# Kernel optimization log

Hardware: AMD Instinct MI355X
Metric: run time of the kernel (lower is better)

Reference implementation:

```python
import jax, jax.numpy as jnp
import numpy as np


def gin_conv(x, src, dst, W, b, num_nodes):
    # PyG GINConv with eps=0: nn((1+eps)*x + sum_{j in N(i)} x_j)
    agg = jax.ops.segment_sum(x[src], dst, num_segments=num_nodes)
    return (x + agg) @ W + b


def setup_inputs() -> dict:
    key = jax.random.key(0)
    ks = jax.random.split(key, 16)
    N, E, F, G = 100000, 3200000, 64, 512
    x = jax.random.normal(ks[0], (N, F), dtype=jnp.float32)
    edge_index = jax.random.randint(ks[1], (2, E), 0, N, dtype=jnp.int64)
    batch = jnp.sort(jax.random.randint(ks[2], (N,), 0, G, dtype=jnp.int64))

    def lin(k, fi, fo):
        return jax.random.normal(k, (fi, fo), dtype=jnp.float32) / np.sqrt(fi)

    return {
        "x": x, "edge_index": edge_index, "batch": batch, "num_graphs": G,
        "W1": lin(ks[3], F, 32), "b1": jnp.zeros((32,), jnp.float32),
        "W2": lin(ks[4], 32, 64), "b2": jnp.zeros((64,), jnp.float32),
        "W3": lin(ks[5], 64, 64), "b3": jnp.zeros((64,), jnp.float32),
        "Wf1": lin(ks[6], 64, 64), "bf1": jnp.zeros((64,), jnp.float32),
        "Wf2": lin(ks[7], 64, 32), "bf2": jnp.zeros((32,), jnp.float32),
        "Wf3": lin(ks[8], 32, 1), "bf3": jnp.zeros((1,), jnp.float32),
    }


def reference(x, edge_index, batch, num_graphs,
              W1, b1, W2, b2, W3, b3, Wf1, bf1, Wf2, bf2, Wf3, bf3):
    N = x.shape[0]
    src, dst = edge_index[0], edge_index[1]
    h = jax.nn.elu(gin_conv(x, src, dst, W1, b1, N))
    h = jax.nn.elu(gin_conv(h, src, dst, W2, b2, N))
    h = jax.nn.elu(gin_conv(h, src, dst, W3, b3, N))
    # scatter_mean pooling over graphs
    sums = jax.ops.segment_sum(h, batch, num_segments=num_graphs)
    cnts = jax.ops.segment_sum(jnp.ones((N,), h.dtype), batch, num_segments=num_graphs)
    g = sums / jnp.maximum(cnts, 1.0)[:, None]
    g = jax.nn.elu(g @ Wf1 + bf1)
    g = jax.nn.elu(g @ Wf2 + bf2)
    g = g @ Wf3 + bf3
    return g.reshape(-1)
```

## Files before the change

### kernel.cpp

```cpp
#include <hip/hip_runtime.h>
#include <hip/hip_bf16.h>


typedef float f4 __attribute__((ext_vector_type(4)));

#define NCHUNK 512
#define MAXK 1024

__device__ __forceinline__ float elu_f(float x) {
  return x > 0.0f ? x : expm1f(x);
}

__device__ __forceinline__ float rl(float v, int q) {
  return __int_as_float(__builtin_amdgcn_readlane(__float_as_int(v), q));
}

__device__ __forceinline__ unsigned short f2bf(float f) {
  unsigned int u = __float_as_uint(f);
  u = (u + 0x7FFFu + ((u >> 16) & 1u)) >> 16;
  return (unsigned short)u;
}

__device__ __forceinline__ void acc_add8(float* a, const uint4 w) {
  a[0] += __uint_as_float(w.x << 16);
  a[1] += __uint_as_float(w.x & 0xffff0000u);
  a[2] += __uint_as_float(w.y << 16);
  a[3] += __uint_as_float(w.y & 0xffff0000u);
  a[4] += __uint_as_float(w.z << 16);
  a[5] += __uint_as_float(w.z & 0xffff0000u);
  a[6] += __uint_as_float(w.w << 16);
  a[7] += __uint_as_float(w.w & 0xffff0000u);
}


__global__ __launch_bounds__(256) void cvt_bf16_kernel(
    const float* __restrict__ in, unsigned short* __restrict__ out, int n4) {
  typedef unsigned short us4 __attribute__((ext_vector_type(4)));
  const int stride = gridDim.x * blockDim.x;
  for (int i = blockIdx.x * blockDim.x + threadIdx.x; i < n4; i += stride) {
    const f4 v = *reinterpret_cast<const f4*>(in + (long long)i * 4);
    us4 o;
    o.x = f2bf(v.x); o.y = f2bf(v.y); o.z = f2bf(v.z); o.w = f2bf(v.w);
    *reinterpret_cast<us4*>(out + (long long)i * 4) = o;
  }
}


__global__ __launch_bounds__(256) void bucket_hist_kernel(
    const int* __restrict__ dst, int* __restrict__ bhist, int E, int K, int chunk) {
  __shared__ int h[MAXK];
  for (int k = threadIdx.x; k < K; k += 256) h[k] = 0;
  __syncthreads();
  const int base = blockIdx.x * chunk;
  const int end = min(E, base + chunk);
  for (int e = base + threadIdx.x; e < end; e += 256)
    atomicAdd(&h[dst[e] >> 7], 1);
  __syncthreads();
  int* row = bhist + (long long)blockIdx.x * K;
  for (int k = threadIdx.x; k < K; k += 256) row[k] = h[k];
}

__global__ __launch_bounds__(NCHUNK) void chunk_scan_kernel(
    const int* __restrict__ bhist, int* __restrict__ cursors,
    int* __restrict__ btot, int K) {
  const int k = blockIdx.x;
  const int t = threadIdx.x;
  const int lane = t & 63;
  const int wv = t >> 6;
  const int own = bhist[(long long)t * K + k];
  int v = own;
#pragma unroll
  for (int off = 1; off < 64; off <<= 1) {
    int u = __shfl_up(v, off, 64);
    if (lane >= off) v += u;
  }
  __shared__ int wsum[8];
  __shared__ int wpre[8];
  if (lane == 63) wsum[wv] = v;
  __syncthreads();
  if (t == 0) {
    int p = 0;
#pragma unroll
    for (int w = 0; w < 8; ++w) { wpre[w] = p; p += wsum[w]; }
  }
  __syncthreads();
  v += wpre[wv];
  cursors[(long long)t * K + k] = v - own;
  if (t == NCHUNK - 1) btot[k] = v;
}

__global__ __launch_bounds__(1024) void bucket_scan_kernel(
    const int* __restrict__ btot, int* __restrict__ bstart, int K) {
  __shared__ int s[1024];
  const int t = threadIdx.x;
  const int own = (t < K) ? btot[t] : 0;
  s[t] = own;
  __syncthreads();
#pragma unroll
  for (int off = 1; off < 1024; off <<= 1) {
    int v = (t >= off) ? s[t - off] : 0;
    __syncthreads();
    s[t] += v;
    __syncthreads();
  }
  if (t < K) bstart[t] = s[t] - own;
  if (t == K - 1) bstart[K] = s[t];
}

__global__ __launch_bounds__(256) void bucket_scatter_kernel(
    const int* __restrict__ src, const int* __restrict__ dst,
    const int* __restrict__ cursors, const int* __restrict__ bstart,
    int* __restrict__ packed, int E, int K, int chunk) {
  __shared__ int cur[MAXK];
  const int c = blockIdx.x;
  for (int k = threadIdx.x; k < K; k += 256)
    cur[k] = cursors[(long long)c * K + k] + bstart[k];
  __syncthreads();
  const int base = c * chunk;
  const int end = min(E, base + chunk);
  for (int e = base + threadIdx.x; e < end; e += 256) {
    const int d = dst[e];
    const int k = d >> 7;
    const int p = atomicAdd(&cur[k], 1);
    packed[p] = ((d & 127) << 18) | src[e];
  }
}

__global__ __launch_bounds__(256) void bucket_sort_kernel(
    const int* __restrict__ packed, const int* __restrict__ bstart,
    int* __restrict__ rowptr, int* __restrict__ eidx, int N, int E, int K) {
  __shared__ int hcnt[128];
  __shared__ int ccur[128];
  __shared__ int wtot;
  const int k = blockIdx.x;
  const int t = threadIdx.x;
  const int lane = t & 63;
  const int n0 = k << 7;
  const int e0 = bstart[k];
  const int e1 = bstart[k + 1];
  if (t < 128) hcnt[t] = 0;
  __syncthreads();
  for (int e = e0 + t; e < e1; e += 256)
    atomicAdd(&hcnt[packed[e] >> 18], 1);
  __syncthreads();
  int v = 0, own = 0;
  if (t < 128) {
    own = hcnt[t];
    v = own;
#pragma unroll
    for (int off = 1; off < 64; off <<= 1) {
      int u = __shfl_up(v, off, 64);
      if (lane >= off) v += u;
    }
  }
  if (t == 63) wtot = v;
  __syncthreads();
  if (t >= 64 && t < 128) v += wtot;
  if (t < 128) {
    const int excl = v - own;
    ccur[t] = excl;
    if (n0 + t < N) rowptr[n0 + t] = e0 + excl;
  }
  if (k == 0 && t == 0) rowptr[N] = E;
  __syncthreads();
  for (int e = e0 + t; e < e1; e += 256) {
    const int w = packed[e];
    const int dl = w >> 18;
    const int p = atomicAdd(&ccur[dl], 1);
    eidx[e0 + p] = w & 0x3FFFF;
  }
}


template <int FO>
__global__ __launch_bounds__(256) void gin_layer64_kernel(
    const unsigned short* __restrict__ h, const int* __restrict__ rowptr,
    const int* __restrict__ eidx, const float* __restrict__ W,
    const float* __restrict__ b, unsigned short* __restrict__ out, int N) {
  const int lane = threadIdx.x & 63;
  const int grp = lane >> 3;
  const int li = lane & 7;
  const int wid = blockIdx.x * (blockDim.x >> 6) + (threadIdx.x >> 6);
  const int nw = gridDim.x * (blockDim.x >> 6);
  const int fo = lane & (FO - 1);
  float wcol[(FO == 32) ? 32 : 64];
  if constexpr (FO == 32) {
    const int kbase = (lane >> 5) * 32;
#pragma unroll
    for (int j = 0; j < 32; ++j) wcol[j] = W[(kbase + j) * 32 + fo];
  } else {
#pragma unroll
    for (int k = 0; k < 64; ++k) wcol[k] = W[k * 64 + fo];
  }
  const float bias = b[fo];

  for (int n = wid; n < N; n += nw) {
    const int r0 = rowptr[n];
    const int cnt = rowptr[n + 1] - r0;
    float a[8] = {0.f, 0.f, 0.f, 0.f, 0.f, 0.f, 0.f, 0.f};
    float a2[8] = {0.f, 0.f, 0.f, 0.f, 0.f, 0.f, 0.f, 0.f};
    int i = grp;
    for (; i + 8 < cnt; i += 16) {
      const int s0 = eidx[r0 + i];
      const int s1 = eidx[r0 + i + 8];
      const uint4 w0 = *reinterpret_cast<const uint4*>(h + (long long)s0 * 64 + li * 8);
      const uint4 w1 = *reinterpret_cast<const uint4*>(h + (long long)s1 * 64 + li * 8);
      acc_add8(a, w0);
      acc_add8(a2, w1);
    }
    if (i < cnt) {
      const int s = eidx[r0 + i];
      acc_add8(a, *reinterpret_cast<const uint4*>(h + (long long)s * 64 + li * 8));
    }
#pragma unroll
    for (int j = 0; j < 8; ++j) {
      a[j] += a2[j];
      a[j] += __shfl_xor(a[j], 8, 64);
      a[j] += __shfl_xor(a[j], 16, 64);
      a[j] += __shfl_xor(a[j], 32, 64);
    }
    acc_add8(a, *reinterpret_cast<const uint4*>(h + (long long)n * 64 + li * 8));
    if constexpr (FO == 32) {
      float o = (lane < 32) ? bias : 0.0f;
      const int pbase = (lane >> 5) * 16;
#pragma unroll
      for (int j = 0; j < 32; ++j) {
        const float av = __int_as_float(__builtin_amdgcn_ds_bpermute(
            pbase + (j >> 3) * 4, __float_as_int(a[j & 7])));
        o = fmaf(av, wcol[j], o);
      }
      o += __shfl_xor(o, 32, 64);
      if (lane < 32) out[(long long)n * 32 + lane] = f2bf(elu_f(o));
    } else {
      float o0 = bias, o1 = 0.0f;
#pragma unroll
      for (int k = 0; k < 64; k += 2) {
        o0 = fmaf(rl(a[k & 7], k >> 3), wcol[k], o0);
        o1 = fmaf(rl(a[(k + 1) & 7], (k + 1) >> 3), wcol[k + 1], o1);
      }
      out[(long long)n * 64 + lane] = f2bf(elu_f(o0 + o1));
    }
  }
}

__global__ __launch_bounds__(256) void gin_layer32_kernel(
    const unsigned short* __restrict__ h, const int* __restrict__ rowptr,
    const int* __restrict__ eidx, const float* __restrict__ W,
    const float* __restrict__ b, unsigned short* __restrict__ out, int N) {
  const int lane = threadIdx.x & 63;
  const int grp = lane >> 2;
  const int li = lane & 3;
  const int wid = blockIdx.x * (blockDim.x >> 6) + (threadIdx.x >> 6);
  const int nw = gridDim.x * (blockDim.x >> 6);
  float wcol[32];
#pragma unroll
  for (int k = 0; k < 32; ++k) wcol[k] = W[k * 64 + lane];
  const float bias = b[lane];

  for (int n = wid; n < N; n += nw) {
    const int r0 = rowptr[n];
    const int cnt = rowptr[n + 1] - r0;
    float a[8] = {0.f, 0.f, 0.f, 0.f, 0.f, 0.f, 0.f, 0.f};
    float a2[8] = {0.f, 0.f, 0.f, 0.f, 0.f, 0.f, 0.f, 0.f};
    int i = grp;
    for (; i + 16 < cnt; i += 32) {
      const int s0 = eidx[r0 + i];
      const int s1 = eidx[r0 + i + 16];
      const uint4 w0 = *reinterpret_cast<const uint4*>(h + (long long)s0 * 32 + li * 8);
      const uint4 w1 = *reinterpret_cast<const uint4*>(h + (long long)s1 * 32 + li * 8);
      acc_add8(a, w0);
      acc_add8(a2, w1);
    }
    if (i < cnt) {
      const int s = eidx[r0 + i];
      acc_add8(a, *reinterpret_cast<const uint4*>(h + (long long)s * 32 + li * 8));
    }
#pragma unroll
    for (int j = 0; j < 8; ++j) {
      a[j] += a2[j];
      a[j] += __shfl_xor(a[j], 4, 64);
      a[j] += __shfl_xor(a[j], 8, 64);
      a[j] += __shfl_xor(a[j], 16, 64);
      a[j] += __shfl_xor(a[j], 32, 64);
    }
    acc_add8(a, *reinterpret_cast<const uint4*>(h + (long long)n * 32 + li * 8));
    float o0 = bias, o1 = 0.0f;
#pragma unroll
    for (int k = 0; k < 32; k += 2) {
      o0 = fmaf(rl(a[k & 7], k >> 3), wcol[k], o0);
      o1 = fmaf(rl(a[(k + 1) & 7], (k + 1) >> 3), wcol[k + 1], o1);
    }
    out[(long long)n * 64 + lane] = f2bf(elu_f(o0 + o1));
  }
}


__global__ void pool_kernel(const unsigned short* __restrict__ h,
                            const int* __restrict__ batch,
                            float* __restrict__ sums,
                            float* __restrict__ cnts,
                            int N) {
  const int groupsPerBlock = blockDim.x >> 6;
  const int grp = blockIdx.x * groupsPerBlock + (threadIdx.x >> 6);
  const int ngrp = gridDim.x * groupsPerBlock;
  const int f = threadIdx.x & 63;
  const int chunk = (N + ngrp - 1) / ngrp;
  const int n0 = grp * chunk;
  const int n1 = min(N, n0 + chunk);
  if (n0 >= n1) return;
  int g = batch[n0];
  float acc = 0.0f;
  float cnt = 0.0f;
  for (int n = n0; n < n1; ++n) {
    const int bg = batch[n];
    if (bg != g) {
      atomicAdd(&sums[(long long)g * 64 + f], acc);
      if (f == 0) atomicAdd(&cnts[g], cnt);
      acc = 0.0f;
      cnt = 0.0f;
      g = bg;
    }
    acc += __uint_as_float((unsigned int)h[(long long)n * 64 + f] << 16);
    cnt += 1.0f;
  }
  atomicAdd(&sums[(long long)g * 64 + f], acc);
  if (f == 0) atomicAdd(&cnts[g], cnt);
}

__global__ void head_kernel(const float* __restrict__ sums,
                            const float* __restrict__ cnts,
                            const float* __restrict__ Wf1, const float* __restrict__ bf1,
                            const float* __restrict__ Wf2, const float* __restrict__ bf2,
                            const float* __restrict__ Wf3, const float* __restrict__ bf3,
                            float* __restrict__ out, int G) {
  __shared__ float s0[64];
  __shared__ float s1[64];
  __shared__ float s2[32];
  const int g = blockIdx.x;
  const int t = threadIdx.x;
  const float c = fmaxf(cnts[g], 1.0f);
  s0[t] = sums[(long long)g * 64 + t] / c;
  __syncthreads();
  float acc = bf1[t];
#pragma unroll
  for (int k = 0; k < 64; ++k) acc += s0[k] * Wf1[k * 64 + t];
  s1[t] = elu_f(acc);
  __syncthreads();
  if (t < 32) {
    float a2 = bf2[t];
#pragma unroll
    for (int k = 0; k < 64; ++k) a2 += s1[k] * Wf2[k * 32 + t];
    s2[t] = elu_f(a2) * Wf3[t];
  }
  __syncthreads();
  if (t == 0) {
    float r = bf3[0];
#pragma unroll
    for (int k = 0; k < 32; ++k) r += s2[k];
    out[g] = r;
  }
}

extern "C" void kernel_launch(void* const* d_in, const int* in_sizes, int n_in,
                              void* d_out, int out_size, void* d_ws, size_t ws_size,
                              hipStream_t stream) {
  const float* x   = (const float*)d_in[0];
  const int* ei    = (const int*)d_in[1];
  const int* batch = (const int*)d_in[2];
  const float* W1  = (const float*)d_in[4];
  const float* b1  = (const float*)d_in[5];
  const float* W2  = (const float*)d_in[6];
  const float* b2  = (const float*)d_in[7];
  const float* W3  = (const float*)d_in[8];
  const float* b3  = (const float*)d_in[9];
  const float* Wf1 = (const float*)d_in[10];
  const float* bf1 = (const float*)d_in[11];
  const float* Wf2 = (const float*)d_in[12];
  const float* bf2 = (const float*)d_in[13];
  const float* Wf3 = (const float*)d_in[14];
  const float* bf3 = (const float*)d_in[15];

  const int N = in_sizes[0] / 64;
  const int E = in_sizes[1] / 2;
  const int G = out_size;
  const int* src = ei;
  const int* dst = ei + E;
  const int K = (N + 127) >> 7;
  const int chunk = (E + NCHUNK - 1) / NCHUNK;

  char* ws = (char*)d_ws;
  size_t off = 0;
  auto alloc = [&](size_t bytes) -> void* {
    void* p = ws + off;
    off = (off + bytes + 255) & ~(size_t)255;
    return p;
  };
  int* bhist   = (int*)alloc((size_t)NCHUNK * K * 4);
  int* cursors = (int*)alloc((size_t)NCHUNK * K * 4);
  int* btot    = (int*)alloc((size_t)K * 4);
  int* bstart  = (int*)alloc((size_t)(K + 1) * 4);
  int* rowptr  = (int*)alloc((size_t)(N + 1) * 4);
  int* eidx    = (int*)alloc((size_t)E * 4);
  int* packed  = (int*)alloc((size_t)E * 4);
  unsigned short* xb = (unsigned short*)alloc((size_t)N * 64 * 2);
  unsigned short* hA = (unsigned short*)alloc((size_t)N * 64 * 2);
  unsigned short* hB = (unsigned short*)alloc((size_t)N * 64 * 2);
  float* sums  = (float*)alloc((size_t)G * 65 * 4);
  float* cnts  = sums + (size_t)G * 64;
  float* out   = (float*)d_out;

  cvt_bf16_kernel<<<1024, 256, 0, stream>>>(x, xb, N * 16);

  bucket_hist_kernel<<<NCHUNK, 256, 0, stream>>>(dst, bhist, E, K, chunk);
  chunk_scan_kernel<<<K, NCHUNK, 0, stream>>>(bhist, cursors, btot, K);
  bucket_scan_kernel<<<1, 1024, 0, stream>>>(btot, bstart, K);
  bucket_scatter_kernel<<<NCHUNK, 256, 0, stream>>>(src, dst, cursors, bstart,
                                                    packed, E, K, chunk);
  bucket_sort_kernel<<<K, 256, 0, stream>>>(packed, bstart, rowptr, eidx, N, E, K);

  gin_layer64_kernel<32><<<2048, 256, 0, stream>>>(xb, rowptr, eidx, W1, b1, hA, N);
  gin_layer32_kernel<<<2048, 256, 0, stream>>>(hA, rowptr, eidx, W2, b2, hB, N);
  gin_layer64_kernel<64><<<2048, 256, 0, stream>>>(hB, rowptr, eidx, W3, b3, hA, N);

  hipMemsetAsync(sums, 0, (size_t)G * 65 * 4, stream);
  pool_kernel<<<512, 256, 0, stream>>>(hA, batch, sums, cnts, N);
  head_kernel<<<G, 64, 0, stream>>>(sums, cnts, Wf1, bf1, Wf2, bf2, Wf3, bf3, out, G);
}
```

Before: 477.1 us.

## Partition edges by source tile so gather passes stay cache-resident

The CSR sort now orders each destination's edges by one of four source-node tiles and produces a 4x rowptr. The GIN layers process each tile in turn, with blocks owning fixed node ranges and keeping partial sums in shared memory between tiles. The goal is to keep the active slice of the source feature table resident in L2/LLC and cut random-gather misses. The cost is extra passes, block barriers, a shared-memory round-trip, and the loss of the dual-accumulator unrolling. The 32-feature layer also switches to 8 lanes of 4 features.

Result: slower. 790.1 us (+65.6%).

```diff
diff --git a/kernel.cpp b/kernel.cpp
--- a/kernel.cpp
+++ b/kernel.cpp
@@ -6,6 +6,7 @@
 
 #define NCHUNK 512
 #define MAXK 1024
+#define T_TILES 4
 
 __device__ __forceinline__ float elu_f(float x) {
   return x > 0.0f ? x : expm1f(x);
@@ -32,6 +33,17 @@
   a[7] += __uint_as_float(w.w & 0xffff0000u);
 }
 
+__device__ __forceinline__ void acc_add4(float* a, const uint2 w) {
+  a[0] += __uint_as_float(w.x << 16);
+  a[1] += __uint_as_float(w.x & 0xffff0000u);
+  a[2] += __uint_as_float(w.y << 16);
+  a[3] += __uint_as_float(w.y & 0xffff0000u);
+}
+
+__device__ __forceinline__ int tile_of(int srcn, float tszInv) {
+  return min(T_TILES - 1, (int)((float)srcn * tszInv));
+}
+
 
 __global__ __launch_bounds__(256) void cvt_bf16_kernel(
     const float* __restrict__ in, unsigned short* __restrict__ out, int n4) {
@@ -128,60 +140,72 @@
 
 __global__ __launch_bounds__(256) void bucket_sort_kernel(
     const int* __restrict__ packed, const int* __restrict__ bstart,
-    int* __restrict__ rowptr, int* __restrict__ eidx, int N, int E, int K) {
-  __shared__ int hcnt[128];
-  __shared__ int ccur[128];
-  __shared__ int wtot;
+    int* __restrict__ rowptr2, int* __restrict__ eidx, int N, int E, int K,
+    float tszInv) {
+  __shared__ int hcnt[512];
+  __shared__ int ccur[512];
+  __shared__ int wsum[4];
   const int k = blockIdx.x;
   const int t = threadIdx.x;
   const int lane = t & 63;
+  const int wv = t >> 6;
   const int n0 = k << 7;
   const int e0 = bstart[k];
   const int e1 = bstart[k + 1];
-  if (t < 128) hcnt[t] = 0;
-  __syncthreads();
-  for (int e = e0 + t; e < e1; e += 256)
-    atomicAdd(&hcnt[packed[e] >> 18], 1);
-  __syncthreads();
-  int v = 0, own = 0;
-  if (t < 128) {
-    own = hcnt[t];
-    v = own;
-#pragma unroll
-    for (int off = 1; off < 64; off <<= 1) {
-      int u = __shfl_up(v, off, 64);
-      if (lane >= off) v += u;
-    }
-  }
-  if (t == 63) wtot = v;
-  __syncthreads();
-  if (t >= 64 && t < 128) v += wtot;
-  if (t < 128) {
-    const int excl = v - own;
-    ccur[t] = excl;
-    if (n0 + t < N) rowptr[n0 + t] = e0 + excl;
-  }
-  if (k == 0 && t == 0) rowptr[N] = E;
+  hcnt[t] = 0;
+  hcnt[t + 256] = 0;
   __syncthreads();
   for (int e = e0 + t; e < e1; e += 256) {
     const int w = packed[e];
-    const int dl = w >> 18;
-    const int p = atomicAdd(&ccur[dl], 1);
-    eidx[e0 + p] = w & 0x3FFFF;
-  }
-}
-
-
-template <int FO>
-__global__ __launch_bounds__(256) void gin_layer64_kernel(
-    const unsigned short* __restrict__ h, const int* __restrict__ rowptr,
+    const int srcn = w & 0x3FFFF;
+    atomicAdd(&hcnt[(w >> 18) * T_TILES + tile_of(srcn, tszInv)], 1);
+  }
+  __syncthreads();
+  const int c0 = hcnt[2 * t];
+  const int c1 = hcnt[2 * t + 1];
+  const int own = c0 + c1;
+  int v = own;
+#pragma unroll
+  for (int off = 1; off < 64; off <<= 1) {
+    int u = __shfl_up(v, off, 64);
+    if (lane >= off) v += u;
+  }
+  if (lane == 63) wsum[wv] = v;
+  __syncthreads();
+  int pre = 0;
+#pragma unroll
+  for (int w = 0; w < 4; ++w) pre += (w < wv) ? wsum[w] : 0;
+  const int ex = pre + v - own;
+  ccur[2 * t] = ex;
+  ccur[2 * t + 1] = ex + c0;
+  const int key0 = 2 * t;
+  const int key1 = 2 * t + 1;
+  if (n0 + (key0 >> 2) < N) rowptr2[(n0 << 2) + key0] = e0 + ex;
+  if (n0 + (key1 >> 2) < N) rowptr2[(n0 << 2) + key1] = e0 + ex + c0;
+  if (k == 0 && t == 0) rowptr2[(long long)N << 2] = E;
+  __syncthreads();
+  for (int e = e0 + t; e < e1; e += 256) {
+    const int w = packed[e];
+    const int srcn = w & 0x3FFFF;
+    const int key = (w >> 18) * T_TILES + tile_of(srcn, tszInv);
+    const int p = atomicAdd(&ccur[key], 1);
+    eidx[e0 + p] = srcn;
+  }
+}
+
+
+template <int FO, int NPB>
+__global__ __launch_bounds__(256) void gin64_tiled_kernel(
+    const unsigned short* __restrict__ h, const int* __restrict__ rp2,
     const int* __restrict__ eidx, const float* __restrict__ W,
     const float* __restrict__ b, unsigned short* __restrict__ out, int N) {
+  __shared__ float accs[NPB][64];
   const int lane = threadIdx.x & 63;
+  const int wv = threadIdx.x >> 6;
   const int grp = lane >> 3;
   const int li = lane & 7;
-  const int wid = blockIdx.x * (blockDim.x >> 6) + (threadIdx.x >> 6);
-  const int nw = gridDim.x * (blockDim.x >> 6);
+  const int nb0 = blockIdx.x * NPB;
+  const int nEnd = min(N, nb0 + NPB);
   const int fo = lane & (FO - 1);
   float wcol[(FO == 32) ? 32 : 64];
   if constexpr (FO == 32) {
@@ -194,103 +218,125 @@
   }
   const float bias = b[fo];
 
-  for (int n = wid; n < N; n += nw) {
-    const int r0 = rowptr[n];
-    const int cnt = rowptr[n + 1] - r0;
-    float a[8] = {0.f, 0.f, 0.f, 0.f, 0.f, 0.f, 0.f, 0.f};
-    float a2[8] = {0.f, 0.f, 0.f, 0.f, 0.f, 0.f, 0.f, 0.f};
-    int i = grp;
-    for (; i + 8 < cnt; i += 16) {
-      const int s0 = eidx[r0 + i];
-      const int s1 = eidx[r0 + i + 8];
-      const uint4 w0 = *reinterpret_cast<const uint4*>(h + (long long)s0 * 64 + li * 8);
-      const uint4 w1 = *reinterpret_cast<const uint4*>(h + (long long)s1 * 64 + li * 8);
-      acc_add8(a, w0);
-      acc_add8(a2, w1);
+#pragma unroll 1
+  for (int tl = 0; tl < T_TILES; ++tl) {
+    for (int nn = nb0 + wv; nn < nEnd; nn += 4) {
+      float a[8];
+      if (tl > 0 && grp == 0) {
+        const f4 p0 = *reinterpret_cast<const f4*>(&accs[nn - nb0][li * 8]);
+        const f4 p1 = *reinterpret_cast<const f4*>(&accs[nn - nb0][li * 8 + 4]);
+        a[0] = p0.x; a[1] = p0.y; a[2] = p0.z; a[3] = p0.w;
+        a[4] = p1.x; a[5] = p1.y; a[6] = p1.z; a[7] = p1.w;
+      } else {
+#pragma unroll
+        for (int j = 0; j < 8; ++j) a[j] = 0.0f;
+      }
+      const int rb = (nn << 2) + tl;
+      const int r0 = rp2[rb];
+      const int r1 = rp2[rb + 1];
+      for (int i = r0 + grp; i < r1; i += 8) {
+        const int s = __builtin_nontemporal_load(&eidx[i]);
+        acc_add8(a, *reinterpret_cast<const uint4*>(h + (long long)s * 64 + li * 8));
+      }
+#pragma unroll
+      for (int j = 0; j < 8; ++j) {
+        a[j] += __shfl_xor(a[j], 8, 64);
+        a[j] += __shfl_xor(a[j], 16, 64);
+        a[j] += __shfl_xor(a[j], 32, 64);
+      }
+      if (tl < T_TILES - 1) {
+        if (grp == 0) {
+          f4 p0 = {a[0], a[1], a[2], a[3]};
+          f4 p1 = {a[4], a[5], a[6], a[7]};
+          *reinterpret_cast<f4*>(&accs[nn - nb0][li * 8]) = p0;
+          *reinterpret_cast<f4*>(&accs[nn - nb0][li * 8 + 4]) = p1;
+        }
+      } else {
+        acc_add8(a, *reinterpret_cast<const uint4*>(h + (long long)nn * 64 + li * 8));
+        if constexpr (FO == 32) {
+          float o = (lane < 32) ? bias : 0.0f;
+          const int pbase = (lane >> 5) * 16;
+#pragma unroll
+          for (int j = 0; j < 32; ++j) {
+            const float av = __int_as_float(__builtin_amdgcn_ds_bpermute(
+                pbase + (j >> 3) * 4, __float_as_int(a[j & 7])));
+            o = fmaf(av, wcol[j], o);
+          }
+          o += __shfl_xor(o, 32, 64);
+          if (lane < 32) out[(long long)nn * 32 + lane] = f2bf(elu_f(o));
+        } else {
+          float o0 = bias, o1 = 0.0f;
+#pragma unroll
+          for (int k2 = 0; k2 < 64; k2 += 2) {
+            o0 = fmaf(rl(a[k2 & 7], k2 >> 3), wcol[k2], o0);
+            o1 = fmaf(rl(a[(k2 + 1) & 7], (k2 + 1) >> 3), wcol[k2 + 1], o1);
+          }
+          out[(long long)nn * 64 + lane] = f2bf(elu_f(o0 + o1));
+        }
+      }
     }
-    if (i < cnt) {
-      const int s = eidx[r0 + i];
-      acc_add8(a, *reinterpret_cast<const uint4*>(h + (long long)s * 64 + li * 8));
-    }
-#pragma unroll
-    for (int j = 0; j < 8; ++j) {
-      a[j] += a2[j];
-      a[j] += __shfl_xor(a[j], 8, 64);
-      a[j] += __shfl_xor(a[j], 16, 64);
-      a[j] += __shfl_xor(a[j], 32, 64);
-    }
-    acc_add8(a, *reinterpret_cast<const uint4*>(h + (long long)n * 64 + li * 8));
-    if constexpr (FO == 32) {
-      float o = (lane < 32) ? bias : 0.0f;
-      const int pbase = (lane >> 5) * 16;
-#pragma unroll
-      for (int j = 0; j < 32; ++j) {
-        const float av = __int_as_float(__builtin_amdgcn_ds_bpermute(
-            pbase + (j >> 3) * 4, __float_as_int(a[j & 7])));
-        o = fmaf(av, wcol[j], o);
-      }
-      o += __shfl_xor(o, 32, 64);
-      if (lane < 32) out[(long long)n * 32 + lane] = f2bf(elu_f(o));
-    } else {
-      float o0 = bias, o1 = 0.0f;
-#pragma unroll
-      for (int k = 0; k < 64; k += 2) {
-        o0 = fmaf(rl(a[k & 7], k >> 3), wcol[k], o0);
-        o1 = fmaf(rl(a[(k + 1) & 7], (k + 1) >> 3), wcol[k + 1], o1);
-      }
-      out[(long long)n * 64 + lane] = f2bf(elu_f(o0 + o1));
-    }
-  }
-}
-
-__global__ __launch_bounds__(256) void gin_layer32_kernel(
-    const unsigned short* __restrict__ h, const int* __restrict__ rowptr,
+    __syncthreads();
+  }
+}
+
+template <int NPB>
+__global__ __launch_bounds__(256) void gin32_tiled_kernel(
+    const unsigned short* __restrict__ h, const int* __restrict__ rp2,
     const int* __restrict__ eidx, const float* __restrict__ W,
     const float* __restrict__ b, unsigned short* __restrict__ out, int N) {
+  __shared__ float accs[NPB][32];
   const int lane = threadIdx.x & 63;
-  const int grp = lane >> 2;
-  const int li = lane & 3;
-  const int wid = blockIdx.x * (blockDim.x >> 6) + (threadIdx.x >> 6);
-  const int nw = gridDim.x * (blockDim.x >> 6);
+  const int wv = threadIdx.x >> 6;
+  const int grp = lane >> 3;
+  const int li = lane & 7;
+  const int nb0 = blockIdx.x * NPB;
+  const int nEnd = min(N, nb0 + NPB);
   float wcol[32];
 #pragma unroll
   for (int k = 0; k < 32; ++k) wcol[k] = W[k * 64 + lane];
   const float bias = b[lane];
 
-  for (int n = wid; n < N; n += nw) {
-    const int r0 = rowptr[n];
-    const int cnt = rowptr[n + 1] - r0;
-    float a[8] = {0.f, 0.f, 0.f, 0.f, 0.f, 0.f, 0.f, 0.f};
-    float a2[8] = {0.f, 0.f, 0.f, 0.f, 0.f, 0.f, 0.f, 0.f};
-    int i = grp;
-    for (; i + 16 < cnt; i += 32) {
-      const int s0 = eidx[r0 + i];
-      const int s1 = eidx[r0 + i + 16];
-      const uint4 w0 = *reinterpret_cast<const uint4*>(h + (long long)s0 * 32 + li * 8);
-      const uint4 w1 = *reinterpret_cast<const uint4*>(h + (long long)s1 * 32 + li * 8);
-      acc_add8(a, w0);
-      acc_add8(a2, w1);
+#pragma unroll 1
+  for (int tl = 0; tl < T_TILES; ++tl) {
+    for (int nn = nb0 + wv; nn < nEnd; nn += 4) {
+      float a[4];
+      if (tl > 0 && grp == 0) {
+        const f4 p0 = *reinterpret_cast<const f4*>(&accs[nn - nb0][li * 4]);
+        a[0] = p0.x; a[1] = p0.y; a[2] = p0.z; a[3] = p0.w;
+      } else {
+#pragma unroll
+        for (int j = 0; j < 4; ++j) a[j] = 0.0f;
+      }
+      const int rb = (nn << 2) + tl;
+      const int r0 = rp2[rb];
+      const int r1 = rp2[rb + 1];
+      for (int i = r0 + grp; i < r1; i += 8) {
+        const int s = __builtin_nontemporal_load(&eidx[i]);
+        acc_add4(a, *reinterpret_cast<const uint2*>(h + (long long)s * 32 + li * 4));
+      }
+#pragma unroll
+      for (int j = 0; j < 4; ++j) {
+        a[j] += __shfl_xor(a[j], 8, 64);
+        a[j] += __shfl_xor(a[j], 16, 64);
+        a[j] += __shfl_xor(a[j], 32, 64);
+      }
+      if (tl < T_TILES - 1) {
+        if (grp == 0) {
+          f4 p0 = {a[0], a[1], a[2], a[3]};
+          *reinterpret_cast<f4*>(&accs[nn - nb0][li * 4]) = p0;
+        }
+      } else {
+        acc_add4(a, *reinterpret_cast<const uint2*>(h + (long long)nn * 32 + li * 4));
+        float o0 = bias, o1 = 0.0f;
+#pragma unroll
+        for (int k2 = 0; k2 < 32; k2 += 2) {
+          o0 = fmaf(rl(a[k2 & 3], k2 >> 2), wcol[k2], o0);
+          o1 = fmaf(rl(a[(k2 + 1) & 3], (k2 + 1) >> 2), wcol[k2 + 1], o1);
+        }
+        out[(long long)nn * 64 + lane] = f2bf(elu_f(o0 + o1));
+      }
     }
-    if (i < cnt) {
-      const int s = eidx[r0 + i];
-      acc_add8(a, *reinterpret_cast<const uint4*>(h + (long long)s * 32 + li * 8));
-    }
-#pragma unroll
-    for (int j = 0; j < 8; ++j) {
-      a[j] += a2[j];
-      a[j] += __shfl_xor(a[j], 4, 64);
-      a[j] += __shfl_xor(a[j], 8, 64);
-      a[j] += __shfl_xor(a[j], 16, 64);
-      a[j] += __shfl_xor(a[j], 32, 64);
-    }
-    acc_add8(a, *reinterpret_cast<const uint4*>(h + (long long)n * 32 + li * 8));
-    float o0 = bias, o1 = 0.0f;
-#pragma unroll
-    for (int k = 0; k < 32; k += 2) {
-      o0 = fmaf(rl(a[k & 7], k >> 3), wcol[k], o0);
-      o1 = fmaf(rl(a[(k + 1) & 7], (k + 1) >> 3), wcol[k + 1], o1);
-    }
-    out[(long long)n * 64 + lane] = f2bf(elu_f(o0 + o1));
+    __syncthreads();
   }
 }
 
@@ -387,6 +433,8 @@
   const int* dst = ei + E;
   const int K = (N + 127) >> 7;
   const int chunk = (E + NCHUNK - 1) / NCHUNK;
+  const int tsz = (N + T_TILES - 1) / T_TILES;
+  const float tszInv = 1.0f / (float)tsz;
 
   char* ws = (char*)d_ws;
   size_t off = 0;
@@ -399,7 +447,7 @@
   int* cursors = (int*)alloc((size_t)NCHUNK * K * 4);
   int* btot    = (int*)alloc((size_t)K * 4);
   int* bstart  = (int*)alloc((size_t)(K + 1) * 4);
-  int* rowptr  = (int*)alloc((size_t)(N + 1) * 4);
+  int* rowptr2 = (int*)alloc(((size_t)N * T_TILES + 1) * 4);
   int* eidx    = (int*)alloc((size_t)E * 4);
   int* packed  = (int*)alloc((size_t)E * 4);
   unsigned short* xb = (unsigned short*)alloc((size_t)N * 64 * 2);
@@ -416,11 +464,17 @@
   bucket_scan_kernel<<<1, 1024, 0, stream>>>(btot, bstart, K);
   bucket_scatter_kernel<<<NCHUNK, 256, 0, stream>>>(src, dst, cursors, bstart,
                                                     packed, E, K, chunk);
-  bucket_sort_kernel<<<K, 256, 0, stream>>>(packed, bstart, rowptr, eidx, N, E, K);
-
-  gin_layer64_kernel<32><<<2048, 256, 0, stream>>>(xb, rowptr, eidx, W1, b1, hA, N);
-  gin_layer32_kernel<<<2048, 256, 0, stream>>>(hA, rowptr, eidx, W2, b2, hB, N);
-  gin_layer64_kernel<64><<<2048, 256, 0, stream>>>(hB, rowptr, eidx, W3, b3, hA, N);
+  bucket_sort_kernel<<<K, 256, 0, stream>>>(packed, bstart, rowptr2, eidx,
+                                            N, E, K, tszInv);
+
+  {
+    const int npb1 = 56, g1 = (N + npb1 - 1) / npb1;
+    gin64_tiled_kernel<32, 56><<<g1, 256, 0, stream>>>(xb, rowptr2, eidx, W1, b1, hA, N);
+    const int npb2 = 56, g2 = (N + npb2 - 1) / npb2;
+    gin32_tiled_kernel<56><<<g2, 256, 0, stream>>>(hA, rowptr2, eidx, W2, b2, hB, N);
+    const int npb3 = 100, g3 = (N + npb3 - 1) / npb3;
+    gin64_tiled_kernel<64, 100><<<g3, 256, 0, stream>>>(hB, rowptr2, eidx, W3, b3, hA, N);
+  }
 
   hipMemsetAsync(sums, 0, (size_t)G * 65 * 4, stream);
   pool_kernel<<<512, 256, 0, stream>>>(hA, batch, sums, cnts, N);
```

## Apply first layer's linear transform before aggregation to halve gather width

Applied to the files above, without the earlier changes.

Uses linearity, (x + A x) W = xW + A(xW), so the first GIN layer multiplies x by W1 up front (64→32 features, stored as bf16) instead of converting x to bf16. The first aggregation then gathers 32-wide rows instead of 64-wide and only adds bias and applies ELU per element. This roughly halves the random-gather traffic of layer one. In exchange it adds a dense GEMM pass over x and changes where bf16 rounding happens.

After: 461.7 us. -3.2%, faster.

```diff
diff --git a/kernel.cpp b/kernel.cpp
--- a/kernel.cpp
+++ b/kernel.cpp
@@ -33,15 +33,29 @@
 }
 
 
-__global__ __launch_bounds__(256) void cvt_bf16_kernel(
-    const float* __restrict__ in, unsigned short* __restrict__ out, int n4) {
-  typedef unsigned short us4 __attribute__((ext_vector_type(4)));
-  const int stride = gridDim.x * blockDim.x;
-  for (int i = blockIdx.x * blockDim.x + threadIdx.x; i < n4; i += stride) {
-    const f4 v = *reinterpret_cast<const f4*>(in + (long long)i * 4);
-    us4 o;
-    o.x = f2bf(v.x); o.y = f2bf(v.y); o.z = f2bf(v.z); o.w = f2bf(v.w);
-    *reinterpret_cast<us4*>(out + (long long)i * 4) = o;
+__global__ __launch_bounds__(256) void gemm1_kernel(
+    const float* __restrict__ x, const float* __restrict__ W,
+    unsigned short* __restrict__ y, int N) {
+  const int lane = threadIdx.x & 63;
+  const int wid = blockIdx.x * 4 + (threadIdx.x >> 6);
+  const int nw = gridDim.x * 4;
+  const int fo = lane & 31;
+  float wcol[64];
+#pragma unroll
+  for (int k = 0; k < 64; ++k) wcol[k] = W[k * 32 + fo];
+  for (int n = wid; n < N; n += nw) {
+    float a[4] = {0.f, 0.f, 0.f, 0.f};
+    if (lane < 16) {
+      const f4 v = *reinterpret_cast<const f4*>(x + (long long)n * 64 + lane * 4);
+      a[0] = v.x; a[1] = v.y; a[2] = v.z; a[3] = v.w;
+    }
+    float o0 = 0.f, o1 = 0.f;
+#pragma unroll
+    for (int k = 0; k < 64; k += 2) {
+      o0 = fmaf(rl(a[k & 3], k >> 2), wcol[k], o0);
+      o1 = fmaf(rl(a[(k + 1) & 3], (k + 1) >> 2), wcol[k + 1], o1);
+    }
+    if (lane < 32) y[(long long)n * 32 + lane] = f2bf(o0 + o1);
   }
 }
 
@@ -172,7 +186,112 @@
 }
 
 
-template <int FO>
+__global__ __launch_bounds__(256) void gin_layer32_elem_kernel(
+    const unsigned short* __restrict__ h, const int* __restrict__ rowptr,
+    const int* __restrict__ eidx, const float* __restrict__ b,
+    unsigned short* __restrict__ out, int N) {
+  const int lane = threadIdx.x & 63;
+  const int grp = lane >> 2;
+  const int li = lane & 3;
+  const int wid = blockIdx.x * (blockDim.x >> 6) + (threadIdx.x >> 6);
+  const int nw = gridDim.x * (blockDim.x >> 6);
+  float bb[8];
+#pragma unroll
+  for (int j = 0; j < 8; ++j) bb[j] = b[li * 8 + j];
+
+  for (int n = wid; n < N; n += nw) {
+    const int r0 = rowptr[n];
+    const int cnt = rowptr[n + 1] - r0;
+    float a[8] = {0.f, 0.f, 0.f, 0.f, 0.f, 0.f, 0.f, 0.f};
+    float a2[8] = {0.f, 0.f, 0.f, 0.f, 0.f, 0.f, 0.f, 0.f};
+    int i = grp;
+    for (; i + 16 < cnt; i += 32) {
+      const int s0 = eidx[r0 + i];
+      const int s1 = eidx[r0 + i + 16];
+      const uint4 w0 = *reinterpret_cast<const uint4*>(h + (long long)s0 * 32 + li * 8);
+      const uint4 w1 = *reinterpret_cast<const uint4*>(h + (long long)s1 * 32 + li * 8);
+      acc_add8(a, w0);
+      acc_add8(a2, w1);
+    }
+    if (i < cnt) {
+      const int s = eidx[r0 + i];
+      acc_add8(a, *reinterpret_cast<const uint4*>(h + (long long)s * 32 + li * 8));
+    }
+#pragma unroll
+    for (int j = 0; j < 8; ++j) {
+      a[j] += a2[j];
+      a[j] += __shfl_xor(a[j], 4, 64);
+      a[j] += __shfl_xor(a[j], 8, 64);
+      a[j] += __shfl_xor(a[j], 16, 64);
+      a[j] += __shfl_xor(a[j], 32, 64);
+    }
+    acc_add8(a, *reinterpret_cast<const uint4*>(h + (long long)n * 32 + li * 8));
+    if (grp == 0) {
+      uint4 o;
+      o.x = (unsigned int)f2bf(elu_f(a[0] + bb[0])) |
+            ((unsigned int)f2bf(elu_f(a[1] + bb[1])) << 16);
+      o.y = (unsigned int)f2bf(elu_f(a[2] + bb[2])) |
+            ((unsigned int)f2bf(elu_f(a[3] + bb[3])) << 16);
+      o.z = (unsigned int)f2bf(elu_f(a[4] + bb[4])) |
+            ((unsigned int)f2bf(elu_f(a[5] + bb[5])) << 16);
+      o.w = (unsigned int)f2bf(elu_f(a[6] + bb[6])) |
+            ((unsigned int)f2bf(elu_f(a[7] + bb[7])) << 16);
+      *reinterpret_cast<uint4*>(out + (long long)n * 32 + li * 8) = o;
+    }
+  }
+}
+
+__global__ __launch_bounds__(256) void gin_layer32_kernel(
+    const unsigned short* __restrict__ h, const int* __restrict__ rowptr,
+    const int* __restrict__ eidx, const float* __restrict__ W,
+    const float* __restrict__ b, unsigned short* __restrict__ out, int N) {
+  const int lane = threadIdx.x & 63;
+  const int grp = lane >> 2;
+  const int li = lane & 3;
+  const int wid = blockIdx.x * (blockDim.x >> 6) + (threadIdx.x >> 6);
+  const int nw = gridDim.x * (blockDim.x >> 6);
+  float wcol[32];
+#pragma unroll
+  for (int k = 0; k < 32; ++k) wcol[k] = W[k * 64 + lane];
+  const float bias = b[lane];
+
+  for (int n = wid; n < N; n += nw) {
+    const int r0 = rowptr[n];
+    const int cnt = rowptr[n + 1] - r0;
+    float a[8] = {0.f, 0.f, 0.f, 0.f, 0.f, 0.f, 0.f, 0.f};
+    float a2[8] = {0.f, 0.f, 0.f, 0.f, 0.f, 0.f, 0.f, 0.f};
+    int i = grp;
+    for (; i + 16 < cnt; i += 32) {
+      const int s0 = eidx[r0 + i];
+      const int s1 = eidx[r0 + i + 16];
+      const uint4 w0 = *reinterpret_cast<const uint4*>(h + (long long)s0 * 32 + li * 8);
+      const uint4 w1 = *reinterpret_cast<const uint4*>(h + (long long)s1 * 32 + li * 8);
+      acc_add8(a, w0);
+      acc_add8(a2, w1);
+    }
+    if (i < cnt) {
+      const int s = eidx[r0 + i];
+      acc_add8(a, *reinterpret_cast<const uint4*>(h + (long long)s * 32 + li * 8));
+    }
+#pragma unroll
+    for (int j = 0; j < 8; ++j) {
+      a[j] += a2[j];
+      a[j] += __shfl_xor(a[j], 4, 64);
+      a[j] += __shfl_xor(a[j], 8, 64);
+      a[j] += __shfl_xor(a[j], 16, 64);
+      a[j] += __shfl_xor(a[j], 32, 64);
+    }
+    acc_add8(a, *reinterpret_cast<const uint4*>(h + (long long)n * 32 + li * 8));
+    float o0 = bias, o1 = 0.0f;
+#pragma unroll
+    for (int k = 0; k < 32; k += 2) {
+      o0 = fmaf(rl(a[k & 7], k >> 3), wcol[k], o0);
+      o1 = fmaf(rl(a[(k + 1) & 7], (k + 1) >> 3), wcol[k + 1], o1);
+    }
+    out[(long long)n * 64 + lane] = f2bf(elu_f(o0 + o1));
+  }
+}
+
 __global__ __launch_bounds__(256) void gin_layer64_kernel(
     const unsigned short* __restrict__ h, const int* __restrict__ rowptr,
     const int* __restrict__ eidx, const float* __restrict__ W,
@@ -182,17 +301,10 @@
   const int li = lane & 7;
   const int wid = blockIdx.x * (blockDim.x >> 6) + (threadIdx.x >> 6);
   const int nw = gridDim.x * (blockDim.x >> 6);
-  const int fo = lane & (FO - 1);
-  float wcol[(FO == 32) ? 32 : 64];
-  if constexpr (FO == 32) {
-    const int kbase = (lane >> 5) * 32;
-#pragma unroll
-    for (int j = 0; j < 32; ++j) wcol[j] = W[(kbase + j) * 32 + fo];
-  } else {
-#pragma unroll
-    for (int k = 0; k < 64; ++k) wcol[k] = W[k * 64 + fo];
-  }
-  const float bias = b[fo];
+  float wcol[64];
+#pragma unroll
+  for (int k = 0; k < 64; ++k) wcol[k] = W[k * 64 + lane];
+  const float bias = b[lane];
 
   for (int n = wid; n < N; n += nw) {
     const int r0 = rowptr[n];
@@ -220,73 +332,9 @@
       a[j] += __shfl_xor(a[j], 32, 64);
     }
     acc_add8(a, *reinterpret_cast<const uint4*>(h + (long long)n * 64 + li * 8));
-    if constexpr (FO == 32) {
-      float o = (lane < 32) ? bias : 0.0f;
-      const int pbase = (lane >> 5) * 16;
-#pragma unroll
-      for (int j = 0; j < 32; ++j) {
-        const float av = __int_as_float(__builtin_amdgcn_ds_bpermute(
-            pbase + (j >> 3) * 4, __float_as_int(a[j & 7])));
-        o = fmaf(av, wcol[j], o);
-      }
-      o += __shfl_xor(o, 32, 64);
-      if (lane < 32) out[(long long)n * 32 + lane] = f2bf(elu_f(o));
-    } else {
-      float o0 = bias, o1 = 0.0f;
-#pragma unroll
-      for (int k = 0; k < 64; k += 2) {
-        o0 = fmaf(rl(a[k & 7], k >> 3), wcol[k], o0);
-        o1 = fmaf(rl(a[(k + 1) & 7], (k + 1) >> 3), wcol[k + 1], o1);
-      }
-      out[(long long)n * 64 + lane] = f2bf(elu_f(o0 + o1));
-    }
-  }
-}
-
-__global__ __launch_bounds__(256) void gin_layer32_kernel(
-    const unsigned short* __restrict__ h, const int* __restrict__ rowptr,
-    const int* __restrict__ eidx, const float* __restrict__ W,
-    const float* __restrict__ b, unsigned short* __restrict__ out, int N) {
-  const int lane = threadIdx.x & 63;
-  const int grp = lane >> 2;
-  const int li = lane & 3;
-  const int wid = blockIdx.x * (blockDim.x >> 6) + (threadIdx.x >> 6);
-  const int nw = gridDim.x * (blockDim.x >> 6);
-  float wcol[32];
-#pragma unroll
-  for (int k = 0; k < 32; ++k) wcol[k] = W[k * 64 + lane];
-  const float bias = b[lane];
-
-  for (int n = wid; n < N; n += nw) {
-    const int r0 = rowptr[n];
-    const int cnt = rowptr[n + 1] - r0;
-    float a[8] = {0.f, 0.f, 0.f, 0.f, 0.f, 0.f, 0.f, 0.f};
-    float a2[8] = {0.f, 0.f, 0.f, 0.f, 0.f, 0.f, 0.f, 0.f};
-    int i = grp;
-    for (; i + 16 < cnt; i += 32) {
-      const int s0 = eidx[r0 + i];
-      const int s1 = eidx[r0 + i + 16];
-      const uint4 w0 = *reinterpret_cast<const uint4*>(h + (long long)s0 * 32 + li * 8);
-      const uint4 w1 = *reinterpret_cast<const uint4*>(h + (long long)s1 * 32 + li * 8);
-      acc_add8(a, w0);
-      acc_add8(a2, w1);
-    }
-    if (i < cnt) {
-      const int s = eidx[r0 + i];
-      acc_add8(a, *reinterpret_cast<const uint4*>(h + (long long)s * 32 + li * 8));
-    }
-#pragma unroll
-    for (int j = 0; j < 8; ++j) {
-      a[j] += a2[j];
-      a[j] += __shfl_xor(a[j], 4, 64);
-      a[j] += __shfl_xor(a[j], 8, 64);
-      a[j] += __shfl_xor(a[j], 16, 64);
-      a[j] += __shfl_xor(a[j], 32, 64);
-    }
-    acc_add8(a, *reinterpret_cast<const uint4*>(h + (long long)n * 32 + li * 8));
     float o0 = bias, o1 = 0.0f;
 #pragma unroll
-    for (int k = 0; k < 32; k += 2) {
+    for (int k = 0; k < 64; k += 2) {
       o0 = fmaf(rl(a[k & 7], k >> 3), wcol[k], o0);
       o1 = fmaf(rl(a[(k + 1) & 7], (k + 1) >> 3), wcol[k + 1], o1);
     }
@@ -402,14 +450,14 @@
   int* rowptr  = (int*)alloc((size_t)(N + 1) * 4);
   int* eidx    = (int*)alloc((size_t)E * 4);
   int* packed  = (int*)alloc((size_t)E * 4);
-  unsigned short* xb = (unsigned short*)alloc((size_t)N * 64 * 2);
+  unsigned short* y1 = (unsigned short*)alloc((size_t)N * 32 * 2);
   unsigned short* hA = (unsigned short*)alloc((size_t)N * 64 * 2);
   unsigned short* hB = (unsigned short*)alloc((size_t)N * 64 * 2);
   float* sums  = (float*)alloc((size_t)G * 65 * 4);
   float* cnts  = sums + (size_t)G * 64;
   float* out   = (float*)d_out;
 
-  cvt_bf16_kernel<<<1024, 256, 0, stream>>>(x, xb, N * 16);
+  gemm1_kernel<<<1024, 256, 0, stream>>>(x, W1, y1, N);
 
   bucket_hist_kernel<<<NCHUNK, 256, 0, stream>>>(dst, bhist, E, K, chunk);
   chunk_scan_kernel<<<K, NCHUNK, 0, stream>>>(bhist, cursors, btot, K);
@@ -418,9 +466,9 @@
                                                     packed, E, K, chunk);
   bucket_sort_kernel<<<K, 256, 0, stream>>>(packed, bstart, rowptr, eidx, N, E, K);
 
-  gin_layer64_kernel<32><<<2048, 256, 0, stream>>>(xb, rowptr, eidx, W1, b1, hA, N);
+  gin_layer32_elem_kernel<<<2048, 256, 0, stream>>>(y1, rowptr, eidx, b1, hA, N);
   gin_layer32_kernel<<<2048, 256, 0, stream>>>(hA, rowptr, eidx, W2, b2, hB, N);
-  gin_layer64_kernel<64><<<2048, 256, 0, stream>>>(hB, rowptr, eidx, W3, b3, hA, N);
+  gin_layer64_kernel<<<2048, 256, 0, stream>>>(hB, rowptr, eidx, W3, b3, hA, N);
 
   hipMemsetAsync(sums, 0, (size_t)G * 65 * 4, stream);
   pool_kernel<<<512, 256, 0, stream>>>(hA, batch, sums, cnts, N);
```
